# Performance work log

Measured on AMD Instinct MI355X. Metric: run time of the kernel, lower is better.

## Reference

```python
import jax, jax.numpy as jnp
import numpy as np

N = 10000      # number of keypoints / graph nodes
CIN = 512      # in_channels
COUT = 512     # out_channels
KCHEB = 5      # Chebyshev order K
KNN = 20       # k nearest neighbors


def setup_inputs() -> dict:
    key = jax.random.key(0)
    k1, k2, k3, k4 = jax.random.split(key, 4)
    x = jax.random.normal(k1, (1, CIN, N), dtype=jnp.float32)
    position = jax.random.normal(k2, (1, N, 3), dtype=jnp.float32)
    # ChebConv weights: one [CIN, COUT] matrix per Chebyshev order, plus bias
    theta = jax.random.normal(k3, (KCHEB, CIN, COUT), dtype=jnp.float32) / np.float32(np.sqrt(CIN * KCHEB))
    bias = jax.random.normal(k4, (COUT,), dtype=jnp.float32) * 0.01
    return {"x": x, "position": position, "theta": theta, "bias": bias, "knn": KNN}


def reference(x, position, theta, bias, knn):
    # ---- knn_graph(position.squeeze(0), k, flow='target_to_source') ----
    pos = position[0]                       # [N, 3]
    n = pos.shape[0]
    sq = jnp.sum(pos * pos, axis=1)
    d2 = sq[:, None] + sq[None, :] - 2.0 * (pos @ pos.T)   # [N, N] squared dists
    d2 = jnp.where(jnp.eye(n, dtype=bool), jnp.inf, d2)    # exclude self (loop=False)
    _, nbr = jax.lax.top_k(-d2, knn)        # [N, knn] nearest neighbor indices
    # flow='target_to_source' => edge_index = [center, neighbor]
    row = jnp.repeat(jnp.arange(n), knn)    # edge source (center) for ChebConv
    col = nbr.reshape(-1)                   # edge target (neighbor)

    # ---- ChebConv sym normalization, lambda_max=2 => L_hat = -D^-1/2 A D^-1/2 ----
    deg = jnp.zeros((n,), x.dtype).at[row].add(jnp.float32(1.0))
    dis = jnp.where(deg > 0, jax.lax.rsqrt(deg), jnp.float32(0.0))
    w = -dis[row] * dis[col]                # [E] edge weights, zero diagonal

    h = jnp.swapaxes(x, 1, 2)               # [B, N, CIN]

    def prop(t):
        # out[target] += w * t[source]  (sparse L_hat @ t)
        msg = t[:, row, :] * w[None, :, None]
        return jnp.zeros_like(t).at[:, col, :].add(msg)

    # Chebyshev recurrence: Tx0 = h, Tx1 = L_hat h, Tx_k = 2 L_hat Tx_{k-1} - Tx_{k-2}
    Tx0 = h
    out = jnp.einsum('bnc,co->bno', Tx0, theta[0])
    Tx1 = prop(Tx0)
    out = out + jnp.einsum('bnc,co->bno', Tx1, theta[1])
    for k in range(2, theta.shape[0]):
        Tx2 = 2.0 * prop(Tx1) - Tx0
        out = out + jnp.einsum('bnc,co->bno', Tx2, theta[k])
        Tx0, Tx1 = Tx1, Tx2
    out = out + bias
    return jnp.swapaxes(out, 1, 2)          # [B, COUT, N]
```

## Files before the change

kernel.cpp:

```cpp
#include <hip/hip_runtime.h>
#include <hip/hip_bf16.h>
#include <cstdint>
#include <cstddef>

#define N_NODES 10000
#define KNN_K 20
#define NEDGE (N_NODES * KNN_K)
#define NBATCH 157
#define POS4_PAD 10048
#define NCELL 4096
#define NPX 1250
#define GM_PAIRS 316

using bf16x8 = __attribute__((ext_vector_type(8))) short;
using f32x4  = __attribute__((ext_vector_type(4))) float;

__device__ __forceinline__ float bf_lo(unsigned int u) {
  union { unsigned int i; float f; } c; c.i = u << 16; return c.f;
}
__device__ __forceinline__ float bf_hi(unsigned int u) {
  union { unsigned int i; float f; } c; c.i = u & 0xFFFF0000u; return c.f;
}
__device__ __forceinline__ unsigned short f2bf(float f) {
  union { float f; unsigned int i; } c; c.f = f;
  unsigned int u = c.i;
  u += 0x7FFFu + ((u >> 16) & 1u);
  return (unsigned short)(u >> 16);
}

__device__ __forceinline__ void gll16(const void* g, void* l) {
  __builtin_amdgcn_global_load_lds(
      (const __attribute__((address_space(1))) unsigned int*)g,
      (__attribute__((address_space(3))) unsigned int*)l,
      16, 0, 0);
}

__global__ __launch_bounds__(256) void transpose_f32_bf16(
    const float* __restrict__ src0, unsigned short* __restrict__ dst,
    int srows, int scols, int dstride, size_t slice_elems, int dcol_per_slice)
{
  __shared__ float lds[64 * 65];
  const int z = blockIdx.z;
  const float* src = src0 + (size_t)z * slice_elems;
  const int dcol0 = z * dcol_per_slice;
  const int c0 = blockIdx.x * 64;
  const int r0 = blockIdx.y * 64;
  const int tid = threadIdx.x;
#pragma unroll
  for (int q = 0; q < 4; ++q) {
    int unit = q * 256 + tid;
    int rr = unit >> 4;
    int cu = unit & 15;
    int r = r0 + rr, c = c0 + cu * 4;
    float4 v = make_float4(0.f, 0.f, 0.f, 0.f);
    if (r < srows && c + 3 < scols) v = *(const float4*)&src[(size_t)r * scols + c];
    lds[rr * 65 + cu * 4 + 0] = v.x;
    lds[rr * 65 + cu * 4 + 1] = v.y;
    lds[rr * 65 + cu * 4 + 2] = v.z;
    lds[rr * 65 + cu * 4 + 3] = v.w;
  }
  __syncthreads();
#pragma unroll
  for (int q = 0; q < 2; ++q) {
    int unit = q * 256 + tid;
    int cl = unit >> 3;
    int ru = unit & 7;
    int c = c0 + cl;
    if (c < scols) {
      unsigned short tmp[8];
#pragma unroll
      for (int j = 0; j < 8; ++j) tmp[j] = f2bf(lds[(ru * 8 + j) * 65 + cl]);
      uint4 o;
      o.x = (unsigned int)tmp[0] | ((unsigned int)tmp[1] << 16);
      o.y = (unsigned int)tmp[2] | ((unsigned int)tmp[3] << 16);
      o.z = (unsigned int)tmp[4] | ((unsigned int)tmp[5] << 16);
      o.w = (unsigned int)tmp[6] | ((unsigned int)tmp[7] << 16);
      *(uint4*)&dst[(size_t)c * dstride + dcol0 + r0 + ru * 8] = o;
    }
  }
}

__global__ __launch_bounds__(256) void pos4_kernel(
    const float* __restrict__ pos, float4* __restrict__ pos4,
    int* __restrict__ counts, int* __restrict__ cursor,
    int* __restrict__ cellid, int* __restrict__ cellcnt,
    int* __restrict__ nfail)
{
  int c = blockIdx.x * 256 + threadIdx.x;
  if (c == 0) *nfail = 0;
  if (c < POS4_PAD) {
    float4 v;
    if (c < N_NODES) {
      float x = pos[c * 3 + 0], y = pos[c * 3 + 1], z = pos[c * 3 + 2];
      v = make_float4(x, y, z, x * x + y * y + z * z);
      int cx = min(15, max(0, (int)floorf((x + 4.0f) * 2.0f)));
      int cy = min(15, max(0, (int)floorf((y + 4.0f) * 2.0f)));
      int cz = min(15, max(0, (int)floorf((z + 4.0f) * 2.0f)));
      int cell = (cx << 8) | (cy << 4) | cz;
      cellid[c] = cell;
      atomicAdd(&cellcnt[cell], 1);
      counts[c] = 0; cursor[c] = 0;
    } else {
      v = make_float4(0.f, 0.f, 0.f, __builtin_inff());
    }
    pos4[c] = v;
  }
}

__global__ __launch_bounds__(256) void cellscan_kernel(
    const int* __restrict__ cellcnt, int* __restrict__ cellptr)
{
  __shared__ int part[256];
  const int tid = threadIdx.x;
  const int base = tid * 16;
  int cv[16];
  int s = 0;
#pragma unroll
  for (int q = 0; q < 4; ++q) {
    int4 v = *(const int4*)&cellcnt[base + q * 4];
    cv[q * 4 + 0] = v.x; cv[q * 4 + 1] = v.y;
    cv[q * 4 + 2] = v.z; cv[q * 4 + 3] = v.w;
    s += v.x + v.y + v.z + v.w;
  }
  part[tid] = s;
  __syncthreads();
  for (int off = 1; off < 256; off <<= 1) {
    int add = (tid >= off) ? part[tid - off] : 0;
    __syncthreads();
    part[tid] += add;
    __syncthreads();
  }
  int run = part[tid] - s;
#pragma unroll
  for (int q = 0; q < 16; ++q) { cellptr[base + q] = run; run += cv[q]; }
  if (tid == 255) cellptr[NCELL] = run;
}

__global__ __launch_bounds__(256) void perm_kernel(
    const int* __restrict__ cellid, const int* __restrict__ cellptr,
    int* __restrict__ cellcur, int* __restrict__ perm,
    const float4* __restrict__ pos4, float4* __restrict__ pos4s)
{
  int c = blockIdx.x * 256 + threadIdx.x;
  if (c < N_NODES) {
    int cell = cellid[c];
    int p = atomicAdd(&cellcur[cell], 1);
    int slot = cellptr[cell] + p;
    perm[slot] = c;
    pos4s[slot] = pos4[c];
  }
}

__device__ __forceinline__ float knn_dist(float4 pi, float4 s) {
  float dot = fmaf(pi.x, s.x, fmaf(pi.y, s.y, pi.z * s.z));
  return fmaf(-2.0f, dot, pi.w + s.w);
}

__device__ __forceinline__ void insert8(float r[8], float k) {
  asm("v_med3_f32 %0, %1, %2, %3" : "=v"(r[7]) : "v"(k), "v"(r[6]), "v"(r[7]));
  asm("v_med3_f32 %0, %1, %2, %3" : "=v"(r[6]) : "v"(k), "v"(r[5]), "v"(r[6]));
  asm("v_med3_f32 %0, %1, %2, %3" : "=v"(r[5]) : "v"(k), "v"(r[4]), "v"(r[5]));
  asm("v_med3_f32 %0, %1, %2, %3" : "=v"(r[4]) : "v"(k), "v"(r[3]), "v"(r[4]));
  asm("v_med3_f32 %0, %1, %2, %3" : "=v"(r[3]) : "v"(k), "v"(r[2]), "v"(r[3]));
  asm("v_med3_f32 %0, %1, %2, %3" : "=v"(r[2]) : "v"(k), "v"(r[1]), "v"(r[2]));
  asm("v_med3_f32 %0, %1, %2, %3" : "=v"(r[1]) : "v"(k), "v"(r[0]), "v"(r[1]));
  r[0] = fminf(r[0], k);
}

__device__ __forceinline__ float merge_tau20(float r[8], int lane) {
  const float INF = __builtin_inff();
  float tau = INF;
#pragma unroll
  for (int t = 0; t < KNN_K; ++t) {
    float m = r[0];
    m = fminf(m, __shfl_xor(m, 1));
    m = fminf(m, __shfl_xor(m, 2));
    m = fminf(m, __shfl_xor(m, 4));
    m = fminf(m, __shfl_xor(m, 8));
    m = fminf(m, __shfl_xor(m, 16));
    m = fminf(m, __shfl_xor(m, 32));
    unsigned long long who = __ballot(r[0] == m);
    int srcl = __ffsll(who) - 1;
    if (lane == srcl) {
#pragma unroll
      for (int z = 0; z < 7; ++z) r[z] = r[z + 1];
      r[7] = INF;
    }
    tau = m;
  }
  return tau;
}

__device__ __forceinline__ void emit_hits(
    int i, bool valid, float d, float tau, int cid, int lane, int& cnt,
    int* __restrict__ knn_out)
{
  unsigned long long less = __ballot(valid && d < tau);
  unsigned long long eq   = __ballot(valid && d == tau);
  if (less) {
    if (valid && d < tau) {
      int pos = cnt + (int)__popcll(less & ((1ull << lane) - 1ull));
      if (pos < KNN_K) knn_out[i * KNN_K + pos] = cid;
    }
    cnt += (int)__popcll(less);
  }
  if (eq && cnt < KNN_K) {
    if (valid && d == tau) {
      int pos = cnt + (int)__popcll(eq & ((1ull << lane) - 1ull));
      if (pos < KNN_K) knn_out[i * KNN_K + pos] = cid;
    }
    cnt = min(KNN_K, cnt + (int)__popcll(eq));
  }
}

__global__ __launch_bounds__(256) void knn_try_kernel(
    const float4* __restrict__ pos4, const float4* __restrict__ pos4s,
    const int* __restrict__ perm, const int* __restrict__ cellptr,
    int* __restrict__ knn_out, int* __restrict__ wl, int* __restrict__ nfail)
{
  const int lane = threadIdx.x & 63, wave = threadIdx.x >> 6;
  const int wid = blockIdx.x * 4 + wave;
  const int i = perm[wid];
  const float4 pi = pos4[i];
  const float INF = __builtin_inff();

  const int cx = min(15, max(0, (int)floorf((pi.x + 4.0f) * 2.0f)));
  const int cy = min(15, max(0, (int)floorf((pi.y + 4.0f) * 2.0f)));
  const int cz = min(15, max(0, (int)floorf((pi.z + 4.0f) * 2.0f)));
  const int x0 = max(cx - 1, 0), x1 = min(cx + 1, 15);
  const int y0 = max(cy - 1, 0), y1 = min(cy + 1, 15);
  const int z0 = max(cz - 1, 0), z1 = min(cz + 1, 15);

  float r[8];
#pragma unroll
  for (int q = 0; q < 8; ++q) r[q] = INF;

  for (int X = x0; X <= x1; ++X)
    for (int Y = y0; Y <= y1; ++Y) {
      const int cb = (X << 8) | (Y << 4);
      const int s0 = cellptr[cb + z0], s1 = cellptr[cb + z1 + 1];
      for (int c0 = s0; c0 < s1; c0 += 64) {
        const int slot = c0 + lane;
        const int idx = min(slot, s1 - 1);
        const float4 s = pos4s[idx];
        const int nid = perm[idx];
        float d = knn_dist(pi, s);
        float k = (slot < s1 && nid != i) ? d : INF;
        insert8(r, k);
      }
    }
  float tau = merge_tau20(r, lane);

  float mx = INF, my = INF, mz = INF;
  if (x0 > 0)  mx = pi.x - (x0 * 0.5f - 4.0f);
  if (x1 < 15) mx = fminf(mx, ((x1 + 1) * 0.5f - 4.0f) - pi.x);
  if (y0 > 0)  my = pi.y - (y0 * 0.5f - 4.0f);
  if (y1 < 15) my = fminf(my, ((y1 + 1) * 0.5f - 4.0f) - pi.y);
  if (z0 > 0)  mz = pi.z - (z0 * 0.5f - 4.0f);
  if (z1 < 15) mz = fminf(mz, ((z1 + 1) * 0.5f - 4.0f) - pi.z);
  const float marg = fminf(mx, fminf(my, mz));

  if (tau < marg * marg) {
    int cnt = 0;
    for (int X = x0; X <= x1; ++X)
      for (int Y = y0; Y <= y1; ++Y) {
        const int cb = (X << 8) | (Y << 4);
        const int s0 = cellptr[cb + z0], s1 = cellptr[cb + z1 + 1];
        for (int c0 = s0; c0 < s1; c0 += 64) {
          const int slot = c0 + lane;
          const int idx = min(slot, s1 - 1);
          const float4 s = pos4s[idx];
          const int nid = perm[idx];
          float d = knn_dist(pi, s);
          bool valid = (slot < s1) && (nid != i);
          emit_hits(i, valid, d, tau, nid, lane, cnt, knn_out);
        }
      }
    return;
  }

  if (lane == 0) {
    int slot = atomicAdd(nfail, 1);
    wl[slot] = i;
  }
}

__global__ __launch_bounds__(256) void knn_full_kernel(
    const float4* __restrict__ pos4, const int* __restrict__ wl,
    const int* __restrict__ nfail, int* __restrict__ knn_out)
{
  const int lane = threadIdx.x & 63, wave = threadIdx.x >> 6;
  const int w = blockIdx.x * 4 + wave;
  if (w >= *nfail) return;
  const int i = wl[w];
  const float4 pi = pos4[i];
  const float INF = __builtin_inff();

  float r[8];
#pragma unroll
  for (int q = 0; q < 8; ++q) r[q] = INF;
#pragma unroll 4
  for (int b = 0; b < NBATCH; ++b) {
    const int cid = b * 64 + lane;
    const float4 s = pos4[cid];
    float d = knn_dist(pi, s);
    float k = (cid == i) ? INF : d;
    insert8(r, k);
  }
  float tau = merge_tau20(r, lane);
  int cnt = 0;
  for (int b = 0; b < NBATCH; ++b) {
    const int cid = b * 64 + lane;
    const float4 s = pos4[cid];
    float d = knn_dist(pi, s);
    bool valid = (cid != i);
    emit_hits(i, valid, d, tau, cid, lane, cnt, knn_out);
  }
}

__global__ __launch_bounds__(256) void count_kernel(
    const int* __restrict__ knn, int* __restrict__ counts)
{
  int e = blockIdx.x * 256 + threadIdx.x;
  if (e < NEDGE) atomicAdd(&counts[knn[e]], 1);
}

__global__ __launch_bounds__(256) void scan_kernel(
    const int* __restrict__ counts, int* __restrict__ rptr)
{
  __shared__ int part[256];
  const int tid = threadIdx.x;
  const int base = tid * 40;
  int s = 0;
  int cv[40];
  if (tid < 250) {
#pragma unroll
    for (int q = 0; q < 10; ++q) {
      int4 v = *(const int4*)&counts[base + q * 4];
      cv[q * 4 + 0] = v.x; cv[q * 4 + 1] = v.y;
      cv[q * 4 + 2] = v.z; cv[q * 4 + 3] = v.w;
      s += v.x + v.y + v.z + v.w;
    }
  }
  part[tid] = s;
  __syncthreads();
  for (int off = 1; off < 256; off <<= 1) {
    int add = (tid >= off) ? part[tid - off] : 0;
    __syncthreads();
    part[tid] += add;
    __syncthreads();
  }
  int run = part[tid] - s;
  if (tid < 250) {
#pragma unroll
    for (int q = 0; q < 40; ++q) { rptr[base + q] = run; run += cv[q]; }
  }
  if (tid == 255) rptr[N_NODES] = run;
}

__global__ __launch_bounds__(256) void fill_kernel(
    const int* __restrict__ knn, const int* __restrict__ rptr,
    int* __restrict__ cursor, int* __restrict__ rsrc)
{
  int e = blockIdx.x * 256 + threadIdx.x;
  if (e < NEDGE) {
    int j = knn[e];
    int i = e / KNN_K;
    int p = atomicAdd(&cursor[j], 1);
    rsrc[rptr[j] + p] = i;
  }
}

__global__ __launch_bounds__(256) void sort_kernel(
    const int* __restrict__ rptr, int* __restrict__ rsrc)
{
  const int lane = threadIdx.x & 63, wave = threadIdx.x >> 6;
  const int j = blockIdx.x * 4 + wave;
  const int s0 = rptr[j], s1 = rptr[j + 1], deg = s1 - s0;
  if (deg <= 64) {
    int v = (lane < deg) ? rsrc[s0 + lane] : 0x7FFFFFFF;
#pragma unroll
    for (int k = 2; k <= 64; k <<= 1) {
#pragma unroll
      for (int m = k >> 1; m > 0; m >>= 1) {
        int other = __shfl_xor(v, m);
        bool up = ((lane & k) == 0);
        bool lower = ((lane & m) == 0);
        v = (up == lower) ? min(v, other) : max(v, other);
      }
    }
    if (lane < deg) rsrc[s0 + lane] = v;
  } else if (lane == 0) {
    for (int a = s0 + 1; a < s1; ++a) {
      int v = rsrc[a];
      int b = a - 1;
      while (b >= s0 && rsrc[b] > v) { rsrc[b + 1] = rsrc[b]; --b; }
      rsrc[b + 1] = v;
    }
  }
}

__global__ __launch_bounds__(256) void prop_kernel(
    const unsigned short* __restrict__ tin, const unsigned short* __restrict__ tprev,
    unsigned short* __restrict__ tout, const int* __restrict__ rptr,
    const int* __restrict__ rsrc, const int* __restrict__ perm, float scale2)
{
  const int wave = threadIdx.x >> 6, lane = threadIdx.x & 63;
  const int b = blockIdx.x;
  const int xcd = b & 7, qb = b >> 3;
  const int local = qb * 4 + wave;
  if (local >= NPX) return;
  const int j = perm[xcd * NPX + local];
  const int s0 = rptr[j], s1 = rptr[j + 1];
  const size_t coff = (size_t)lane * 8;

  float a0[8], a1[8], a2[8], a3[8];
#pragma unroll
  for (int q = 0; q < 8; ++q) { a0[q] = 0.f; a1[q] = 0.f; a2[q] = 0.f; a3[q] = 0.f; }

  for (int base = s0; base < s1; base += 64) {
    const int clen = min(64, s1 - base);
    int myidx = (base + lane < s1) ? rsrc[base + lane] : 0;
    int t = 0;
    for (; t + 4 <= clen; t += 4) {
      int i0 = __shfl(myidx, t);
      int i1 = __shfl(myidx, t + 1);
      int i2 = __shfl(myidx, t + 2);
      int i3 = __shfl(myidx, t + 3);
      uint4 v0 = *(const uint4*)&tin[(size_t)i0 * 512 + coff];
      uint4 v1 = *(const uint4*)&tin[(size_t)i1 * 512 + coff];
      uint4 v2 = *(const uint4*)&tin[(size_t)i2 * 512 + coff];
      uint4 v3 = *(const uint4*)&tin[(size_t)i3 * 512 + coff];
      a0[0] += bf_lo(v0.x); a0[1] += bf_hi(v0.x); a0[2] += bf_lo(v0.y); a0[3] += bf_hi(v0.y);
      a0[4] += bf_lo(v0.z); a0[5] += bf_hi(v0.z); a0[6] += bf_lo(v0.w); a0[7] += bf_hi(v0.w);
      a1[0] += bf_lo(v1.x); a1[1] += bf_hi(v1.x); a1[2] += bf_lo(v1.y); a1[3] += bf_hi(v1.y);
      a1[4] += bf_lo(v1.z); a1[5] += bf_hi(v1.z); a1[6] += bf_lo(v1.w); a1[7] += bf_hi(v1.w);
      a2[0] += bf_lo(v2.x); a2[1] += bf_hi(v2.x); a2[2] += bf_lo(v2.y); a2[3] += bf_hi(v2.y);
      a2[4] += bf_lo(v2.z); a2[5] += bf_hi(v2.z); a2[6] += bf_lo(v2.w); a2[7] += bf_hi(v2.w);
      a3[0] += bf_lo(v3.x); a3[1] += bf_hi(v3.x); a3[2] += bf_lo(v3.y); a3[3] += bf_hi(v3.y);
      a3[4] += bf_lo(v3.z); a3[5] += bf_hi(v3.z); a3[6] += bf_lo(v3.w); a3[7] += bf_hi(v3.w);
    }
    for (; t < clen; ++t) {
      int i0 = __shfl(myidx, t);
      uint4 v0 = *(const uint4*)&tin[(size_t)i0 * 512 + coff];
      a0[0] += bf_lo(v0.x); a0[1] += bf_hi(v0.x); a0[2] += bf_lo(v0.y); a0[3] += bf_hi(v0.y);
      a0[4] += bf_lo(v0.z); a0[5] += bf_hi(v0.z); a0[6] += bf_lo(v0.w); a0[7] += bf_hi(v0.w);
    }
  }

  float pv[8] = {0.f, 0.f, 0.f, 0.f, 0.f, 0.f, 0.f, 0.f};
  if (tprev != nullptr) {
    uint4 p = *(const uint4*)&tprev[(size_t)j * 512 + coff];
    pv[0] = bf_lo(p.x); pv[1] = bf_hi(p.x);
    pv[2] = bf_lo(p.y); pv[3] = bf_hi(p.y);
    pv[4] = bf_lo(p.z); pv[5] = bf_hi(p.z);
    pv[6] = bf_lo(p.w); pv[7] = bf_hi(p.w);
  }
  unsigned short o16[8];
#pragma unroll
  for (int q = 0; q < 8; ++q) {
    float acc = (a0[q] + a1[q]) + (a2[q] + a3[q]);
    o16[q] = f2bf(scale2 * acc - pv[q]);
  }
  uint4 o;
  o.x = (unsigned int)o16[0] | ((unsigned int)o16[1] << 16);
  o.y = (unsigned int)o16[2] | ((unsigned int)o16[3] << 16);
  o.z = (unsigned int)o16[4] | ((unsigned int)o16[5] << 16);
  o.w = (unsigned int)o16[6] | ((unsigned int)o16[7] << 16);
  *(uint4*)&tout[(size_t)j * 512 + coff] = o;
}

__global__ __launch_bounds__(256) void gemm_kernel(
    const unsigned short* __restrict__ A,
    const unsigned short* __restrict__ Bt,
    const float* __restrict__ bias,
    float* __restrict__ C)
{
  __shared__ __align__(16) char smem[65536];
  float* eps = (float*)smem;

  const int tid = threadIdx.x;
  const int wave = tid >> 6, lane = tid & 63;
  const int l15 = lane & 15, hi = lane >> 4;
  const int wr = wave >> 1, wc = wave & 1;

  const int bid = blockIdx.x;
  const int xcd = bid & 7, local = bid >> 3;
  const int qd = GM_PAIRS >> 3, rem = GM_PAIRS & 7;
  const int cnt = (xcd < rem) ? qd + 1 : qd;
  if (local >= cnt) return;
  const int start = (xcd < rem) ? xcd * (qd + 1) : rem * (qd + 1) + (xcd - rem) * qd;
  const int pair = start + local;
  const int n0 = (pair >> 2) * 128;
  const int o0 = (pair & 3) * 128;

  f32x4 acc[4][4];
#pragma unroll
  for (int a = 0; a < 4; ++a)
#pragma unroll
    for (int b = 0; b < 4; ++b) acc[a][b] = (f32x4){0.f, 0.f, 0.f, 0.f};

  auto stage = [&](int kt, int sel) {
    const int k0 = kt * 64;
    const int ko = k0 >> 9;
    const int c0 = k0 & 511;
    const unsigned short* Ab = A + (size_t)ko * ((size_t)N_NODES * 512);
    unsigned short* As = (unsigned short*)(smem + sel * 32768);
    unsigned short* Bs = As + 128 * 64;
#pragma unroll
    for (int q = 0; q < 4; ++q) {
      int idx = (wave * 4 + q) * 64 + lane;
      int r = idx >> 3, u = idx & 7;
      int ug = u ^ (r & 7);
      gll16(Ab + (size_t)(n0 + r) * 512 + c0 + ug * 8, As + (size_t)(wave * 4 + q) * 512);
    }
#pragma unroll
    for (int q = 0; q < 4; ++q) {
      int idx = (wave * 4 + q) * 64 + lane;
      int r = idx >> 3, u = idx & 7;
      int ug = u ^ (r & 7);
      gll16(Bt + (size_t)(o0 + r) * 2560 + k0 + ug * 8, Bs + (size_t)(wave * 4 + q) * 512);
    }
  };

  stage(0, 0);
  __syncthreads();

  int cur = 0;
  for (int kt = 0; kt < 40; ++kt) {
    if (kt + 1 < 40) stage(kt + 1, cur ^ 1);
    unsigned short* As = (unsigned short*)(smem + cur * 32768);
    unsigned short* Bs = As + 128 * 64;
#pragma unroll
    for (int kk = 0; kk < 2; ++kk) {
      bf16x8 af[4], bfr[4];
#pragma unroll
      for (int mi = 0; mi < 4; ++mi) {
        int row = wr * 64 + mi * 16 + l15;
        int up = (kk * 4 + hi) ^ (row & 7);
        af[mi] = *(const bf16x8*)(As + row * 64 + up * 8);
      }
#pragma unroll
      for (int ni = 0; ni < 4; ++ni) {
        int row = wc * 64 + ni * 16 + l15;
        int up = (kk * 4 + hi) ^ (row & 7);
        bfr[ni] = *(const bf16x8*)(Bs + row * 64 + up * 8);
      }
#pragma unroll
      for (int mi = 0; mi < 4; ++mi)
#pragma unroll
        for (int ni = 0; ni < 4; ++ni)
          acc[mi][ni] = __builtin_amdgcn_mfma_f32_16x16x32_bf16(af[mi], bfr[ni], acc[mi][ni], 0, 0, 0);
    }
    __syncthreads();
    cur ^= 1;
  }

#pragma unroll
  for (int h = 0; h < 2; ++h) {
    __syncthreads();
    if (wc == h) {
#pragma unroll
      for (int mi = 0; mi < 4; ++mi)
#pragma unroll
        for (int ni = 0; ni < 4; ++ni) {
          int o_l = ni * 16 + l15;
          int nb = wr * 64 + mi * 16 + hi * 4;
          *(f32x4*)&eps[o_l * 132 + nb] = acc[mi][ni];
        }
    }
    __syncthreads();
#pragma unroll
    for (int q = 0; q < 8; ++q) {
      int unit = q * 256 + tid;
      int o_l = unit >> 5, nu = unit & 31;
      int n = n0 + nu * 4;
      if (n < N_NODES) {
        int o = o0 + h * 64 + o_l;
        f32x4 v = *(const f32x4*)&eps[o_l * 132 + nu * 4];
        float bo = bias[o];
        v = v + bo;
        *(f32x4*)&C[(size_t)o * N_NODES + n] = v;
      }
    }
  }
}

extern "C" void kernel_launch(void* const* d_in, const int* in_sizes, int n_in,
                              void* d_out, int out_size, void* d_ws, size_t ws_size,
                              hipStream_t stream)
{
  const float* x        = (const float*)d_in[0];
  const float* position = (const float*)d_in[1];
  const float* theta    = (const float*)d_in[2];
  const float* bias     = (const float*)d_in[3];

  char* ws = (char*)d_ws;
  size_t off = 0;
  auto alloc = [&](size_t bytes) -> void* {
    void* p = ws + off;
    off = (off + bytes + 255) & ~(size_t)255;
    return p;
  };
  unsigned short* TxAll   = (unsigned short*)alloc(5ull * N_NODES * 512 * 2 + 131072);
  unsigned short* thetabT = (unsigned short*)alloc(512ull * 2560 * 2);
  float4* pos4  = (float4*)alloc((size_t)POS4_PAD * 16);
  float4* pos4s = (float4*)alloc((size_t)N_NODES * 16);
  int* knn    = (int*)alloc((size_t)NEDGE * 4);
  int* rptr   = (int*)alloc((size_t)(N_NODES + 1) * 4);
  int* counts = (int*)alloc((size_t)N_NODES * 4);
  int* cursor = (int*)alloc((size_t)N_NODES * 4);
  int* rsrc   = (int*)alloc((size_t)NEDGE * 4);
  int* cellcnt = (int*)alloc((size_t)NCELL * 4);
  int* cellcur = (int*)alloc((size_t)NCELL * 4);
  int* cellptr = (int*)alloc((size_t)(NCELL + 1) * 4);
  int* cellid  = (int*)alloc((size_t)N_NODES * 4);
  int* perm    = (int*)alloc((size_t)N_NODES * 4);
  int* wl      = (int*)alloc((size_t)N_NODES * 4);
  int* nfail   = (int*)alloc(256);
  if (ws_size < off) return;

  transpose_f32_bf16<<<dim3(8, 8, 5), 256, 0, stream>>>(
      theta, thetabT, 512, 512, 2560, (size_t)512 * 512, 512);
  transpose_f32_bf16<<<dim3(157, 8, 1), 256, 0, stream>>>(
      x, TxAll, 512, N_NODES, 512, 0, 0);

  hipMemsetAsync(cellcnt, 0, (size_t)((char*)cellptr - (char*)cellcnt), stream);
  pos4_kernel<<<40, 256, 0, stream>>>(position, pos4, counts, cursor, cellid, cellcnt, nfail);
  cellscan_kernel<<<1, 256, 0, stream>>>(cellcnt, cellptr);
  perm_kernel<<<40, 256, 0, stream>>>(cellid, cellptr, cellcur, perm, pos4, pos4s);

  knn_try_kernel<<<2500, 256, 0, stream>>>(pos4, pos4s, perm, cellptr, knn, wl, nfail);
  knn_full_kernel<<<2500, 256, 0, stream>>>(pos4, wl, nfail, knn);

  count_kernel<<<(NEDGE + 255) / 256, 256, 0, stream>>>(knn, counts);
  scan_kernel<<<1, 256, 0, stream>>>(counts, rptr);
  fill_kernel<<<(NEDGE + 255) / 256, 256, 0, stream>>>(knn, rptr, cursor, rsrc);
  sort_kernel<<<2500, 256, 0, stream>>>(rptr, rsrc);

  unsigned short* Tx0 = TxAll;
  unsigned short* Tx1 = TxAll + 1ull * N_NODES * 512;
  unsigned short* Tx2 = TxAll + 2ull * N_NODES * 512;
  unsigned short* Tx3 = TxAll + 3ull * N_NODES * 512;
  unsigned short* Tx4 = TxAll + 4ull * N_NODES * 512;

  prop_kernel<<<2504, 256, 0, stream>>>(Tx0, nullptr, Tx1, rptr, rsrc, perm, -0.05f);
  prop_kernel<<<2504, 256, 0, stream>>>(Tx1, Tx0,     Tx2, rptr, rsrc, perm, -0.10f);
  prop_kernel<<<2504, 256, 0, stream>>>(Tx2, Tx1,     Tx3, rptr, rsrc, perm, -0.10f);
  prop_kernel<<<2504, 256, 0, stream>>>(Tx3, Tx2,     Tx4, rptr, rsrc, perm, -0.10f);

  gemm_kernel<<<320, 256, 0, stream>>>(TxAll, thetabT, bias, (float*)d_out);
}
```

Before: 249.1 us.

## Spread brute-force KNN fallback for each point across a whole block

The fallback KNN kernel now gives each failed point to a full 256-thread block, striding over the candidates with four waves, instead of one wave per point. The 20th-smallest threshold is found by 20 rounds of block-wide min extraction through shared memory. Hits are emitted with shared-memory atomics, and ties at the threshold go through a sorted buffer. The aim is more parallelism per fallback point, at the cost of many __syncthreads and a launch configuration that must match the stride of 2500.

Result: faster. 231.5 us (-7.0%).

```diff
diff --git a/kernel.cpp b/kernel.cpp
--- a/kernel.cpp
+++ b/kernel.cpp
@@ -289,32 +289,87 @@
     const float4* __restrict__ pos4, const int* __restrict__ wl,
     const int* __restrict__ nfail, int* __restrict__ knn_out)
 {
-  const int lane = threadIdx.x & 63, wave = threadIdx.x >> 6;
-  const int w = blockIdx.x * 4 + wave;
-  if (w >= *nfail) return;
-  const int i = wl[w];
-  const float4 pi = pos4[i];
+  __shared__ float wmin[4];
+  __shared__ int lcnt, eqcnt;
+  __shared__ int eqbuf[64];
+  const int tid = threadIdx.x;
+  const int lane = tid & 63, wave = tid >> 6;
   const float INF = __builtin_inff();
-
-  float r[8];
-#pragma unroll
-  for (int q = 0; q < 8; ++q) r[q] = INF;
-#pragma unroll 4
-  for (int b = 0; b < NBATCH; ++b) {
-    const int cid = b * 64 + lane;
-    const float4 s = pos4[cid];
-    float d = knn_dist(pi, s);
-    float k = (cid == i) ? INF : d;
-    insert8(r, k);
-  }
-  float tau = merge_tau20(r, lane);
-  int cnt = 0;
-  for (int b = 0; b < NBATCH; ++b) {
-    const int cid = b * 64 + lane;
-    const float4 s = pos4[cid];
-    float d = knn_dist(pi, s);
-    bool valid = (cid != i);
-    emit_hits(i, valid, d, tau, cid, lane, cnt, knn_out);
+  const int nf = *nfail;
+
+  for (int w = blockIdx.x; w < nf; w += 2500) {
+    const int i = wl[w];
+    const float4 pi = pos4[i];
+
+    float r[8];
+#pragma unroll
+    for (int q = 0; q < 8; ++q) r[q] = INF;
+    for (int b = wave; b < NBATCH; b += 4) {
+      const int cid = b * 64 + lane;
+      const float4 s = pos4[cid];
+      float d = knn_dist(pi, s);
+      float k = (cid == i) ? INF : d;
+      insert8(r, k);
+    }
+
+    float tau = INF;
+#pragma unroll
+    for (int t = 0; t < KNN_K; ++t) {
+      float m = r[0];
+      m = fminf(m, __shfl_xor(m, 1));
+      m = fminf(m, __shfl_xor(m, 2));
+      m = fminf(m, __shfl_xor(m, 4));
+      m = fminf(m, __shfl_xor(m, 8));
+      m = fminf(m, __shfl_xor(m, 16));
+      m = fminf(m, __shfl_xor(m, 32));
+      if (lane == 0) wmin[wave] = m;
+      __syncthreads();
+      float m0 = wmin[0], m1 = wmin[1], m2 = wmin[2], m3 = wmin[3];
+      float gm = fminf(fminf(m0, m1), fminf(m2, m3));
+      int wsel = (m0 == gm) ? 0 : ((m1 == gm) ? 1 : ((m2 == gm) ? 2 : 3));
+      __syncthreads();
+      if (wave == wsel) {
+        unsigned long long who = __ballot(r[0] == gm);
+        int srcl = __ffsll(who) - 1;
+        if (lane == srcl) {
+#pragma unroll
+          for (int z = 0; z < 7; ++z) r[z] = r[z + 1];
+          r[7] = INF;
+        }
+      }
+      tau = gm;
+    }
+
+    if (tid == 0) { lcnt = 0; eqcnt = 0; }
+    __syncthreads();
+    for (int b = wave; b < NBATCH; b += 4) {
+      const int cid = b * 64 + lane;
+      const float4 s = pos4[cid];
+      float d = knn_dist(pi, s);
+      bool valid = (cid != i);
+      if (valid && d < tau) {
+        int slot = atomicAdd(&lcnt, 1);
+        if (slot < KNN_K) knn_out[i * KNN_K + slot] = cid;
+      }
+      if (valid && d == tau) {
+        int e = atomicAdd(&eqcnt, 1);
+        if (e < 64) eqbuf[e] = cid;
+      }
+    }
+    __syncthreads();
+    if (tid == 0) {
+      int base = lcnt;
+      int ne = min(eqcnt, 64);
+      for (int a = 1; a < ne; ++a) {
+        int v = eqbuf[a];
+        int b2 = a - 1;
+        while (b2 >= 0 && eqbuf[b2] > v) { eqbuf[b2 + 1] = eqbuf[b2]; --b2; }
+        eqbuf[b2 + 1] = v;
+      }
+      for (int q = 0; q < ne && base + q < KNN_K; ++q)
+        knn_out[i * KNN_K + base + q] = eqbuf[q];
+    }
+    __syncthreads();
   }
 }
 
```
